# Performance work log

Hardware: AMD Instinct MI355X
Metric: run time of the kernel (lower is better)

Reference implementation:

```python
import jax, jax.numpy as jnp
import numpy as np

B, S, K, D = 512, 64, 8, 16
NE, NR, NU = 2_000_000, 64, 10_000
NSTEPS, NUNITS, NITER = 100, 128, 2


def _alpha_schedule():
    # betas = sigmoid(linspace(-6,6)) * (0.005 - 1e-5) + 1e-5; alphas_prod = cumprod(1-betas)
    betas = jax.nn.sigmoid(jnp.linspace(-6.0, 6.0, NSTEPS)) * (0.005 - 1e-5) + 1e-5
    aprod = jnp.cumprod(1.0 - betas)
    return jnp.sqrt(aprod), jnp.sqrt(1.0 - aprod)


def _forward(usr_emb, ent_emb, rel_emb, agg_W, agg_b, fc1_W, fc1_b, fc2_W, fc2_b,
             mlp_W1, mlp_b1, mlp_W2, mlp_b2, mlp_W3, mlp_b3, mlp_W4, mlp_b4,
             step_emb1, step_emb2, step_emb3, noise_e, u, v, click_seq, adj_ent, adj_rel, t):
    user = usr_emb[u]                                   # [B,D]
    # --- diffusion branch: x = x0*sqrt(abar_t) + e*sqrt(1-abar_t), then MLP with step-emb adds
    abar_sqrt, ombar_sqrt = _alpha_schedule()
    x = user * abar_sqrt[t][:, None] + noise_e * ombar_sqrt[t][:, None]
    for Wl, bl, se in ((mlp_W1, mlp_b1, step_emb1), (mlp_W2, mlp_b2, step_emb2), (mlp_W3, mlp_b3, step_emb3)):
        x = jax.nn.relu(x @ Wl + bl + se[t])            # [B,128]
    diff_out = x @ mlp_W4 + mlp_b4                      # [B,D]
    # --- multi-hop neighbor gather (entities/relations per hop)
    e0 = click_seq                                      # [B,S]
    e1 = adj_ent[e0]                                    # [B,S,K]
    e2 = adj_ent[e1].reshape(B, S, K * K)               # [B,S,K*K]
    r0 = adj_rel[e0]                                    # [B,S,K]
    r1 = adj_rel[e1].reshape(B, S, K * K)               # [B,S,K*K]
    ev = [ent_emb[e0][:, :, None, :], ent_emb[e1], ent_emb[e2]]  # [B,S,1,D],[B,S,K,D],[B,S,K*K,D]
    rv = [rel_emb[r0], rel_emb[r1]]

    def aggregate(self_v, neigh_v, rel_v, act):
        # KGCN sum-aggregator: user-relation score softmax over neighbors, weighted sum, linear, act
        scores = jnp.mean(user[:, None, None, None, :] * rel_v, axis=-1)   # [B,S,n,K]
        p = jax.nn.softmax(scores, axis=-1)
        neigh_agg = jnp.einsum('bsnk,bsnkd->bsnd', p, neigh_v)             # [B,S,n,D]
        return act((self_v + neigh_agg) @ agg_W + agg_b)

    for i in range(NITER):
        act = jnp.tanh if i == NITER - 1 else jax.nn.sigmoid
        nxt = []
        for hop in range(NITER - i):
            n_self = ev[hop].shape[2]
            nv = ev[hop + 1].reshape(B, S, n_self, K, D)
            relv = rv[hop].reshape(B, S, n_self, K, D)
            nxt.append(aggregate(ev[hop], nv, relv, act))
        ev = nxt
    item_emb = jax.nn.relu(ev[0].reshape(B, S, D))      # relu applied twice in source == once
    trans = item_emb                                    # Transform treated as identity (code unavailable)
    s_sum = jax.nn.relu(jnp.sum(trans, axis=1))         # [B,D]
    s_max = jax.nn.relu(jnp.max(trans, axis=1))         # [B,D]
    fusion = jnp.concatenate([s_sum, s_max], axis=1)    # [B,2D]
    feat = jax.nn.relu(jax.nn.relu(fusion @ fc1_W + fc1_b) @ fc2_W + fc2_b)  # [B,D]
    outs = jax.nn.sigmoid(jnp.sum(feat * ent_emb[v], axis=1))               # [B]
    return jnp.concatenate([outs[:, None], diff_out], axis=1)               # [B,1+D]


def setup_inputs() -> dict:
    key = jax.random.key(0)
    ks = iter(jax.random.split(key, 32))
    nrm = lambda shape, s: jax.random.normal(next(ks), shape, dtype=jnp.float32) * s
    zf = lambda shape: jnp.zeros(shape, dtype=jnp.float32)
    ri = lambda shape, hi: jax.random.randint(next(ks), shape, 0, hi, dtype=jnp.int32)
    return {
        'usr_emb': nrm((NU, D), 0.1), 'ent_emb': nrm((NE, D), 0.1), 'rel_emb': nrm((NR, D), 0.1),
        'agg_W': nrm((D, D), 0.25), 'agg_b': zf((D,)),
        'fc1_W': nrm((2 * D, 64), 0.18), 'fc1_b': zf((64,)),
        'fc2_W': nrm((64, D), 0.125), 'fc2_b': zf((D,)),
        'mlp_W1': nrm((D, NUNITS), 0.25), 'mlp_b1': zf((NUNITS,)),
        'mlp_W2': nrm((NUNITS, NUNITS), 0.09), 'mlp_b2': zf((NUNITS,)),
        'mlp_W3': nrm((NUNITS, NUNITS), 0.09), 'mlp_b3': zf((NUNITS,)),
        'mlp_W4': nrm((NUNITS, D), 0.09), 'mlp_b4': zf((D,)),
        'step_emb1': nrm((NSTEPS, NUNITS), 0.1), 'step_emb2': nrm((NSTEPS, NUNITS), 0.1),
        'step_emb3': nrm((NSTEPS, NUNITS), 0.1),
        'noise_e': jax.random.normal(next(ks), (B, D), dtype=jnp.float32),
        'u': ri((B,), NU), 'v': ri((B,), NE), 'click_seq': ri((B, S), NE),
        'adj_ent': ri((NE, K), NE), 'adj_rel': ri((NE, K), NR), 't': ri((B,), NSTEPS),
    }


def reference(usr_emb, ent_emb, rel_emb, agg_W, agg_b, fc1_W, fc1_b, fc2_W, fc2_b,
              mlp_W1, mlp_b1, mlp_W2, mlp_b2, mlp_W3, mlp_b3, mlp_W4, mlp_b4,
              step_emb1, step_emb2, step_emb3, noise_e, u, v, click_seq, adj_ent, adj_rel, t):
    return _forward(usr_emb, ent_emb, rel_emb, agg_W, agg_b, fc1_W, fc1_b, fc2_W, fc2_b,
                    mlp_W1, mlp_b1, mlp_W2, mlp_b2, mlp_W3, mlp_b3, mlp_W4, mlp_b4,
                    step_emb1, step_emb2, step_emb3, noise_e, u, v, click_seq, adj_ent, adj_rel, t)
```

## Files before the change

### kernel.cpp

```cpp
#include <hip/hip_runtime.h>
#include <math.h>

namespace {
constexpr int B = 512, S = 64, K = 8, D = 16, NR = 64, NSTEPS = 100, NUNITS = 128;
}

#define WAVE_LDS_FENCE() __asm__ volatile("s_waitcnt lgkmcnt(0)" ::: "memory")

__global__ __launch_bounds__(256) void k_prep_all(
    const float* __restrict__ usr_emb, const float* __restrict__ rel_emb,
    const int* __restrict__ u, const int* __restrict__ click_seq,
    const int* __restrict__ adj_ent, const int* __restrict__ adj_rel,
    float* __restrict__ w_tab, int* __restrict__ e1s, int* __restrict__ r0s,
    float* __restrict__ sa, float* __restrict__ so)
{
    int b = blockIdx.x, t = threadIdx.x;
    if (t < 64) {
        const float* ur = usr_emb + (long)u[b] * D;
        const float* rr = rel_emb + t * D;
        float s = 0.f;
#pragma unroll
        for (int d = 0; d < D; ++d) s += ur[d] * rr[d];
        w_tab[b * NR + t] = s * (1.0f / 16.0f);
    } else if (t < 128) {
        int p = b * S + (t - 64);
        int e0 = click_seq[p];
        const int4* ae = (const int4*)(adj_ent + (long)e0 * K);
        const int4* ar = (const int4*)(adj_rel + (long)e0 * K);
        int4 a0 = ae[0], a1 = ae[1], b0 = ar[0], b1 = ar[1];
        int4* oe = (int4*)(e1s + (long)p * K);
        int4* orr = (int4*)(r0s + (long)p * K);
        oe[0] = a0; oe[1] = a1;
        orr[0] = b0; orr[1] = b1;
    } else if (b == 0 && (t - 128) < NSTEPS) {
        int i = t - 128;
        float prod = 1.0f;
        for (int jj = 0; jj <= i; ++jj) {
            float x = -6.0f + (float)jj * (12.0f / 99.0f);
            float sig = 1.0f / (1.0f + expf(-x));
            prod *= (1.0f - (sig * (0.005f - 1e-5f) + 1e-5f));
        }
        sa[i] = sqrtf(prod);
        so[i] = sqrtf(1.0f - prod);
    }
}

__global__ __launch_bounds__(256) void k_kgcn(
    const float* __restrict__ ent_emb,
    const float* __restrict__ w_tab,
    const int* __restrict__ click_seq,
    const int* __restrict__ adj_ent,
    const int* __restrict__ adj_rel,
    const int* __restrict__ e1s,
    const int* __restrict__ r0s,
    const float* __restrict__ agg_W,
    const float* __restrict__ agg_b,
    float* __restrict__ item)
{
    __shared__ float wb[4][NR];
    __shared__ float Ws[4][D][D + 1];
    __shared__ float bs[4][D];
    __shared__ float Ms[4][K][D + 1];
    __shared__ float h1s[4][K][D + 1];
    __shared__ float h0s[4][D];
    __shared__ float A0s[4][D];
    __shared__ float M1s[4][D];
    __shared__ float p0s[4][K];

    const int tid = threadIdx.x;
    const int w = tid >> 6;
    const int lane = tid & 63;
    const int p = blockIdx.x * 4 + w;
    const int b = p >> 6;
    const int k = lane >> 3, j = lane & 7;

    const int e0 = click_seq[p];
    const int e1k = e1s[(long)p * K + k];
    const int r0k = r0s[(long)p * K + k];
    const int e2kj = adj_ent[(long)e1k * K + j];
    const int r1kj = adj_rel[(long)e1k * K + j];

    {
        const float4 wv = ((const float4*)agg_W)[lane];
        int row = lane >> 2, col = (lane & 3) * 4;
        Ws[w][row][col] = wv.x; Ws[w][row][col + 1] = wv.y;
        Ws[w][row][col + 2] = wv.z; Ws[w][row][col + 3] = wv.w;
        wb[w][lane] = w_tab[b * NR + lane];
        if (lane < D) bs[w][lane] = agg_b[lane];
    }
    WAVE_LDS_FENCE();

    float s1 = wb[w][r1kj];
    float m1 = s1;
    m1 = fmaxf(m1, __shfl_xor(m1, 1));
    m1 = fmaxf(m1, __shfl_xor(m1, 2));
    m1 = fmaxf(m1, __shfl_xor(m1, 4));
    float ex = expf(s1 - m1);
    float den = ex;
    den += __shfl_xor(den, 1);
    den += __shfl_xor(den, 2);
    den += __shfl_xor(den, 4);
    float p1 = ex / den;

    float q2r[D], q1r[D], q0r[D];
    {
        const float4* q2p = (const float4*)(ent_emb + (long)e2kj * D);
        float4 a0 = q2p[0], a1 = q2p[1], a2 = q2p[2], a3 = q2p[3];
        q2r[0]=a0.x; q2r[1]=a0.y; q2r[2]=a0.z; q2r[3]=a0.w;
        q2r[4]=a1.x; q2r[5]=a1.y; q2r[6]=a1.z; q2r[7]=a1.w;
        q2r[8]=a2.x; q2r[9]=a2.y; q2r[10]=a2.z; q2r[11]=a2.w;
        q2r[12]=a3.x; q2r[13]=a3.y; q2r[14]=a3.z; q2r[15]=a3.w;
    }
    {
        const float4* q1p = (const float4*)(ent_emb + (long)e1k * D);
        float4 a0 = q1p[0], a1 = q1p[1], a2 = q1p[2], a3 = q1p[3];
        q1r[0]=a0.x; q1r[1]=a0.y; q1r[2]=a0.z; q1r[3]=a0.w;
        q1r[4]=a1.x; q1r[5]=a1.y; q1r[6]=a1.z; q1r[7]=a1.w;
        q1r[8]=a2.x; q1r[9]=a2.y; q1r[10]=a2.z; q1r[11]=a2.w;
        q1r[12]=a3.x; q1r[13]=a3.y; q1r[14]=a3.z; q1r[15]=a3.w;
    }
    {
        const float4* q0p = (const float4*)(ent_emb + (long)e0 * D);
        float4 a0 = q0p[0], a1 = q0p[1], a2 = q0p[2], a3 = q0p[3];
        q0r[0]=a0.x; q0r[1]=a0.y; q0r[2]=a0.z; q0r[3]=a0.w;
        q0r[4]=a1.x; q0r[5]=a1.y; q0r[6]=a1.z; q0r[7]=a1.w;
        q0r[8]=a2.x; q0r[9]=a2.y; q0r[10]=a2.z; q0r[11]=a2.w;
        q0r[12]=a3.x; q0r[13]=a3.y; q0r[14]=a3.z; q0r[15]=a3.w;
    }

    {
        float cur[16];
#pragma unroll
        for (int d = 0; d < 16; ++d) cur[d] = p1 * q2r[d];
        const bool b0 = (lane & 1), b1 = (lane & 2), b2 = (lane & 4);
        float n8[8];
#pragma unroll
        for (int d = 0; d < 8; ++d) {
            float snd = b0 ? cur[d] : cur[d + 8];
            float kp  = b0 ? cur[d + 8] : cur[d];
            n8[d] = kp + __shfl_xor(snd, 1);
        }
        float n4[4];
#pragma unroll
        for (int d = 0; d < 4; ++d) {
            float snd = b1 ? n8[d] : n8[d + 4];
            float kp  = b1 ? n8[d + 4] : n8[d];
            n4[d] = kp + __shfl_xor(snd, 2);
        }
        float a0 = (b2 ? n4[2] : n4[0]) + __shfl_xor(b2 ? n4[0] : n4[2], 4);
        float a1 = (b2 ? n4[3] : n4[1]) + __shfl_xor(b2 ? n4[1] : n4[3], 4);
        const int dbase = (b0 ? 8 : 0) + (b1 ? 4 : 0) + (b2 ? 2 : 0);
        Ms[w][k][dbase]     = q1r[dbase]     + a0;
        Ms[w][k][dbase + 1] = q1r[dbase + 1] + a1;
    }

    float s0 = wb[w][r0k];
    float m0 = s0;
    m0 = fmaxf(m0, __shfl_xor(m0, 8));
    m0 = fmaxf(m0, __shfl_xor(m0, 16));
    m0 = fmaxf(m0, __shfl_xor(m0, 32));
    float e0x = expf(s0 - m0);
    float d0 = e0x;
    d0 += __shfl_xor(d0, 8);
    d0 += __shfl_xor(d0, 16);
    d0 += __shfl_xor(d0, 32);
    float p0 = e0x / d0;
    if (j == 0) p0s[w][k] = p0;

    {
        float cur[16];
#pragma unroll
        for (int d = 0; d < 16; ++d) cur[d] = p0 * q1r[d];
        const bool c0 = (lane & 8), c1 = (lane & 16), c2 = (lane & 32);
        float n8[8];
#pragma unroll
        for (int d = 0; d < 8; ++d) {
            float snd = c0 ? cur[d] : cur[d + 8];
            float kp  = c0 ? cur[d + 8] : cur[d];
            n8[d] = kp + __shfl_xor(snd, 8);
        }
        float n4[4];
#pragma unroll
        for (int d = 0; d < 4; ++d) {
            float snd = c1 ? n8[d] : n8[d + 4];
            float kp  = c1 ? n8[d + 4] : n8[d];
            n4[d] = kp + __shfl_xor(snd, 16);
        }
        float a0 = (c2 ? n4[2] : n4[0]) + __shfl_xor(c2 ? n4[0] : n4[2], 32);
        float a1 = (c2 ? n4[3] : n4[1]) + __shfl_xor(c2 ? n4[1] : n4[3], 32);
        const int dbase = (c0 ? 8 : 0) + (c1 ? 4 : 0) + (c2 ? 2 : 0);
        if (j == 0) { A0s[w][dbase] = a0; A0s[w][dbase + 1] = a1; }
    }
    WAVE_LDS_FENCE();

#pragma unroll
    for (int o = lane; o < 128; o += 64) {
        int ko = o >> 4, dd = o & 15;
        float acc = bs[w][dd];
#pragma unroll
        for (int din = 0; din < D; ++din) acc += Ms[w][ko][din] * Ws[w][din][dd];
        h1s[w][ko][dd] = 1.0f / (1.0f + expf(-acc));
    }

    const int ddl = lane & 15;
    {
        float acc = bs[w][ddl];
#pragma unroll
        for (int din = 0; din < D; ++din)
            acc += (q0r[din] + A0s[w][din]) * Ws[w][din][ddl];
        if (lane < D) h0s[w][lane] = 1.0f / (1.0f + expf(-acc));
    }
    WAVE_LDS_FENCE();

    if (lane < D) {
        float m = h0s[w][lane];
#pragma unroll
        for (int kk = 0; kk < K; ++kk) m += p0s[w][kk] * h1s[w][kk][lane];
        M1s[w][lane] = m;
    }
    WAVE_LDS_FENCE();

    {
        float acc = bs[w][ddl];
#pragma unroll
        for (int din = 0; din < D; ++din) acc += M1s[w][din] * Ws[w][din][ddl];
        if (lane < D) item[(long)p * D + lane] = fmaxf(tanhf(acc), 0.0f);
    }
}

__global__ __launch_bounds__(128) void k_tail(
    const float* __restrict__ item,
    const float* __restrict__ fc1_W, const float* __restrict__ fc1_b,
    const float* __restrict__ fc2_W, const float* __restrict__ fc2_b,
    const float* __restrict__ ent_emb, const int* __restrict__ v,
    const float* __restrict__ usr_emb, const float* __restrict__ noise_e,
    const int* __restrict__ u, const int* __restrict__ t_arr,
    const float* __restrict__ W1, const float* __restrict__ b1,
    const float* __restrict__ W2, const float* __restrict__ b2,
    const float* __restrict__ W3, const float* __restrict__ b3,
    const float* __restrict__ W4, const float* __restrict__ b4,
    const float* __restrict__ se1, const float* __restrict__ se2,
    const float* __restrict__ se3,
    const float* __restrict__ sa, const float* __restrict__ so,
    float* __restrict__ out)
{
    __shared__ float x0[D];
    __shared__ float ha[NUNITS];
    __shared__ float hb[NUNITS];
    __shared__ float sm[S][D + 1];
    __shared__ float fus[2 * D];
    __shared__ float hid[64];
    __shared__ float feat_s[D];

    int b = blockIdx.x, t = threadIdx.x;
    int ts = t_arr[b];

    if (t < D)
        x0[t] = usr_emb[(long)u[b] * D + t] * sa[ts] + noise_e[(long)b * D + t] * so[ts];
    __syncthreads();

    float a = b1[t] + se1[(long)ts * NUNITS + t];
#pragma unroll
    for (int i = 0; i < D; ++i) a += x0[i] * W1[i * NUNITS + t];
    ha[t] = fmaxf(a, 0.0f);
    __syncthreads();

    a = b2[t] + se2[(long)ts * NUNITS + t];
    for (int i = 0; i < NUNITS; ++i) a += ha[i] * W2[i * NUNITS + t];
    hb[t] = fmaxf(a, 0.0f);
    __syncthreads();

    a = b3[t] + se3[(long)ts * NUNITS + t];
    for (int i = 0; i < NUNITS; ++i) a += hb[i] * W3[i * NUNITS + t];
    __syncthreads();
    ha[t] = fmaxf(a, 0.0f);
    __syncthreads();

    if (t < D) {
        float acc = b4[t];
        for (int i = 0; i < NUNITS; ++i) acc += ha[i] * W4[i * D + t];
        out[(long)b * 17 + 1 + t] = acc;
    }

    if (t < 64) {
        const float4* ip = (const float4*)(item + ((long)b * S + t) * D);
        float4 r0 = ip[0], r1 = ip[1], r2 = ip[2], r3 = ip[3];
        sm[t][0]=r0.x;  sm[t][1]=r0.y;  sm[t][2]=r0.z;  sm[t][3]=r0.w;
        sm[t][4]=r1.x;  sm[t][5]=r1.y;  sm[t][6]=r1.z;  sm[t][7]=r1.w;
        sm[t][8]=r2.x;  sm[t][9]=r2.y;  sm[t][10]=r2.z; sm[t][11]=r2.w;
        sm[t][12]=r3.x; sm[t][13]=r3.y; sm[t][14]=r3.z; sm[t][15]=r3.w;
    }
    __syncthreads();

    if (t < D) {
        float sv = 0.0f, mv = -1e30f;
        for (int ss = 0; ss < S; ++ss) {
            float x = sm[ss][t];
            sv += x;
            mv = fmaxf(mv, x);
        }
        fus[t] = fmaxf(sv, 0.0f);
        fus[D + t] = fmaxf(mv, 0.0f);
    }
    __syncthreads();

    if (t < 64) {
        float acc = fc1_b[t];
#pragma unroll
        for (int i = 0; i < 2 * D; ++i) acc += fus[i] * fc1_W[i * 64 + t];
        hid[t] = fmaxf(acc, 0.0f);
    }
    __syncthreads();

    if (t < D) {
        float f = fc2_b[t];
#pragma unroll
        for (int i = 0; i < 64; ++i) f += hid[i] * fc2_W[i * D + t];
        feat_s[t] = fmaxf(f, 0.0f);
    }
    __syncthreads();

    if (t < D) {
        float g = feat_s[t] * ent_emb[(long)v[b] * D + t];
        g += __shfl_xor(g, 1);
        g += __shfl_xor(g, 2);
        g += __shfl_xor(g, 4);
        g += __shfl_xor(g, 8);
        if (t == 0) out[(long)b * 17] = 1.0f / (1.0f + expf(-g));
    }
}

extern "C" void kernel_launch(void* const* d_in, const int* in_sizes, int n_in,
                              void* d_out, int out_size, void* d_ws, size_t ws_size,
                              hipStream_t stream) {
    const float* usr_emb = (const float*)d_in[0];
    const float* ent_emb = (const float*)d_in[1];
    const float* rel_emb = (const float*)d_in[2];
    const float* agg_W   = (const float*)d_in[3];
    const float* agg_b   = (const float*)d_in[4];
    const float* fc1_W   = (const float*)d_in[5];
    const float* fc1_b   = (const float*)d_in[6];
    const float* fc2_W   = (const float*)d_in[7];
    const float* fc2_b   = (const float*)d_in[8];
    const float* mlp_W1  = (const float*)d_in[9];
    const float* mlp_b1  = (const float*)d_in[10];
    const float* mlp_W2  = (const float*)d_in[11];
    const float* mlp_b2  = (const float*)d_in[12];
    const float* mlp_W3  = (const float*)d_in[13];
    const float* mlp_b3  = (const float*)d_in[14];
    const float* mlp_W4  = (const float*)d_in[15];
    const float* mlp_b4  = (const float*)d_in[16];
    const float* se1     = (const float*)d_in[17];
    const float* se2     = (const float*)d_in[18];
    const float* se3     = (const float*)d_in[19];
    const float* noise_e = (const float*)d_in[20];
    const int* u         = (const int*)d_in[21];
    const int* v         = (const int*)d_in[22];
    const int* click_seq = (const int*)d_in[23];
    const int* adj_ent   = (const int*)d_in[24];
    const int* adj_rel   = (const int*)d_in[25];
    const int* t         = (const int*)d_in[26];
    float* out = (float*)d_out;

    float* ws = (float*)d_ws;
    float* w_tab = ws;
    float* sa    = w_tab + B * NR;
    float* so    = sa + 128;
    float* item  = so + 128;
    int*   e1s   = (int*)(item + B * S * D);
    int*   r0s   = e1s + B * S * K;

    k_prep_all<<<B, 256, 0, stream>>>(usr_emb, rel_emb, u, click_seq, adj_ent, adj_rel,
                                      w_tab, e1s, r0s, sa, so);
    k_kgcn<<<(B * S) / 4, 256, 0, stream>>>(ent_emb, w_tab, click_seq, adj_ent, adj_rel,
                                            e1s, r0s, agg_W, agg_b, item);
    k_tail<<<B, 128, 0, stream>>>(item, fc1_W, fc1_b, fc2_W, fc2_b, ent_emb, v,
                                  usr_emb, noise_e, u, t, mlp_W1, mlp_b1, mlp_W2, mlp_b2,
                                  mlp_W3, mlp_b3, mlp_W4, mlp_b4, se1, se2, se3, sa, so, out);
}
```

Measured before the change: 337.4 us.

## Prefetch packed second-hop neighbors in prep kernel and split tail MLP across 256 threads

The prep kernel now also gathers the second-hop adjacency rows for every first-hop neighbor and writes them as packed (entity<<6 | relation) ints. The KGCN kernel reads one coalesced int per lane instead of doing two dependent random gathers into adj_ent and adj_rel. Adjacency loads use nontemporal hints. The tail kernel doubles its threads to split the 128x128 matvecs in half and to overlap the fc branch with the diffusion MLP. The trade-off is extra workspace traffic and more work in the prep kernel.

Result: no change. 334.7 us (-0.8%).

```diff
diff --git a/kernel.cpp b/kernel.cpp
--- a/kernel.cpp
+++ b/kernel.cpp
@@ -3,6 +3,12 @@
 
 namespace {
 constexpr int B = 512, S = 64, K = 8, D = 16, NR = 64, NSTEPS = 100, NUNITS = 128;
+}
+
+typedef int i4 __attribute__((ext_vector_type(4)));
+
+static __device__ __forceinline__ i4 ntload4(const int* p) {
+    return __builtin_nontemporal_load((const i4*)p);
 }
 
 #define WAVE_LDS_FENCE() __asm__ volatile("s_waitcnt lgkmcnt(0)" ::: "memory")
@@ -12,8 +18,10 @@
     const int* __restrict__ u, const int* __restrict__ click_seq,
     const int* __restrict__ adj_ent, const int* __restrict__ adj_rel,
     float* __restrict__ w_tab, int* __restrict__ e1s, int* __restrict__ r0s,
+    int* __restrict__ e2r1,
     float* __restrict__ sa, float* __restrict__ so)
 {
+    __shared__ int e1L[S * K];
     int b = blockIdx.x, t = threadIdx.x;
     if (t < 64) {
         const float* ur = usr_emb + (long)u[b] * D;
@@ -23,15 +31,19 @@
         for (int d = 0; d < D; ++d) s += ur[d] * rr[d];
         w_tab[b * NR + t] = s * (1.0f / 16.0f);
     } else if (t < 128) {
-        int p = b * S + (t - 64);
+        int s = t - 64;
+        int p = b * S + s;
         int e0 = click_seq[p];
-        const int4* ae = (const int4*)(adj_ent + (long)e0 * K);
-        const int4* ar = (const int4*)(adj_rel + (long)e0 * K);
-        int4 a0 = ae[0], a1 = ae[1], b0 = ar[0], b1 = ar[1];
-        int4* oe = (int4*)(e1s + (long)p * K);
-        int4* orr = (int4*)(r0s + (long)p * K);
-        oe[0] = a0; oe[1] = a1;
-        orr[0] = b0; orr[1] = b1;
+        i4 a0 = ntload4(adj_ent + (long)e0 * K);
+        i4 a1 = ntload4(adj_ent + (long)e0 * K + 4);
+        i4 c0 = ntload4(adj_rel + (long)e0 * K);
+        i4 c1 = ntload4(adj_rel + (long)e0 * K + 4);
+        *(i4*)(e1s + (long)p * K)     = a0;
+        *(i4*)(e1s + (long)p * K + 4) = a1;
+        *(i4*)(r0s + (long)p * K)     = c0;
+        *(i4*)(r0s + (long)p * K + 4) = c1;
+        *(i4*)(e1L + s * K)     = a0;
+        *(i4*)(e1L + s * K + 4) = a1;
     } else if (b == 0 && (t - 128) < NSTEPS) {
         int i = t - 128;
         float prod = 1.0f;
@@ -43,16 +55,29 @@
         sa[i] = sqrtf(prod);
         so[i] = sqrtf(1.0f - prod);
     }
+    __syncthreads();
+
+    i4* oer = (i4*)(e2r1 + (long)b * (S * K * K));
+#pragma unroll
+    for (int it = 0; it < 2; ++it) {
+        int idx = t * 2 + it;
+        int e1k = e1L[idx];
+        i4 x0 = ntload4(adj_ent + (long)e1k * K);
+        i4 x1 = ntload4(adj_ent + (long)e1k * K + 4);
+        i4 y0 = ntload4(adj_rel + (long)e1k * K);
+        i4 y1 = ntload4(adj_rel + (long)e1k * K + 4);
+        oer[idx * 2]     = (x0 << 6) | y0;
+        oer[idx * 2 + 1] = (x1 << 6) | y1;
+    }
 }
 
 __global__ __launch_bounds__(256) void k_kgcn(
     const float* __restrict__ ent_emb,
     const float* __restrict__ w_tab,
     const int* __restrict__ click_seq,
-    const int* __restrict__ adj_ent,
-    const int* __restrict__ adj_rel,
     const int* __restrict__ e1s,
     const int* __restrict__ r0s,
+    const int* __restrict__ e2r1,
     const float* __restrict__ agg_W,
     const float* __restrict__ agg_b,
     float* __restrict__ item)
@@ -77,8 +102,9 @@
     const int e0 = click_seq[p];
     const int e1k = e1s[(long)p * K + k];
     const int r0k = r0s[(long)p * K + k];
-    const int e2kj = adj_ent[(long)e1k * K + j];
-    const int r1kj = adj_rel[(long)e1k * K + j];
+    const int pk = __builtin_nontemporal_load(e2r1 + (long)p * (K * K) + lane);
+    const int e2kj = ((unsigned)pk) >> 6;
+    const int r1kj = pk & 63;
 
     {
         const float4 wv = ((const float4*)agg_W)[lane];
@@ -228,7 +254,7 @@
     }
 }
 
-__global__ __launch_bounds__(128) void k_tail(
+__global__ __launch_bounds__(256) void k_tail(
     const float* __restrict__ item,
     const float* __restrict__ fc1_W, const float* __restrict__ fc1_b,
     const float* __restrict__ fc2_W, const float* __restrict__ fc2_b,
@@ -245,89 +271,107 @@
     float* __restrict__ out)
 {
     __shared__ float x0[D];
-    __shared__ float ha[NUNITS];
-    __shared__ float hb[NUNITS];
+    __shared__ float v1[NUNITS], v2[NUNITS], v3[NUNITS];
+    __shared__ float pp[2][NUNITS];
     __shared__ float sm[S][D + 1];
     __shared__ float fus[2 * D];
     __shared__ float hid[64];
     __shared__ float feat_s[D];
 
-    int b = blockIdx.x, t = threadIdx.x;
-    int ts = t_arr[b];
-
-    if (t < D)
-        x0[t] = usr_emb[(long)u[b] * D + t] * sa[ts] + noise_e[(long)b * D + t] * so[ts];
-    __syncthreads();
-
-    float a = b1[t] + se1[(long)ts * NUNITS + t];
-#pragma unroll
-    for (int i = 0; i < D; ++i) a += x0[i] * W1[i * NUNITS + t];
-    ha[t] = fmaxf(a, 0.0f);
-    __syncthreads();
-
-    a = b2[t] + se2[(long)ts * NUNITS + t];
-    for (int i = 0; i < NUNITS; ++i) a += ha[i] * W2[i * NUNITS + t];
-    hb[t] = fmaxf(a, 0.0f);
-    __syncthreads();
-
-    a = b3[t] + se3[(long)ts * NUNITS + t];
-    for (int i = 0; i < NUNITS; ++i) a += hb[i] * W3[i * NUNITS + t];
-    __syncthreads();
-    ha[t] = fmaxf(a, 0.0f);
-    __syncthreads();
-
-    if (t < D) {
-        float acc = b4[t];
-        for (int i = 0; i < NUNITS; ++i) acc += ha[i] * W4[i * D + t];
-        out[(long)b * 17 + 1 + t] = acc;
-    }
-
-    if (t < 64) {
-        const float4* ip = (const float4*)(item + ((long)b * S + t) * D);
+    const int b = blockIdx.x, tid = threadIdx.x;
+    const int t = tid & 127, h = tid >> 7;
+    const int ts = t_arr[b];
+
+    if (tid < D)
+        x0[tid] = usr_emb[(long)u[b] * D + tid] * sa[ts] + noise_e[(long)b * D + tid] * so[ts];
+    if (tid >= 128 && tid < 192) {
+        int ss = tid - 128;
+        const float4* ip = (const float4*)(item + ((long)b * S + ss) * D);
         float4 r0 = ip[0], r1 = ip[1], r2 = ip[2], r3 = ip[3];
-        sm[t][0]=r0.x;  sm[t][1]=r0.y;  sm[t][2]=r0.z;  sm[t][3]=r0.w;
-        sm[t][4]=r1.x;  sm[t][5]=r1.y;  sm[t][6]=r1.z;  sm[t][7]=r1.w;
-        sm[t][8]=r2.x;  sm[t][9]=r2.y;  sm[t][10]=r2.z; sm[t][11]=r2.w;
-        sm[t][12]=r3.x; sm[t][13]=r3.y; sm[t][14]=r3.z; sm[t][15]=r3.w;
-    }
-    __syncthreads();
-
-    if (t < D) {
+        sm[ss][0]=r0.x;  sm[ss][1]=r0.y;  sm[ss][2]=r0.z;  sm[ss][3]=r0.w;
+        sm[ss][4]=r1.x;  sm[ss][5]=r1.y;  sm[ss][6]=r1.z;  sm[ss][7]=r1.w;
+        sm[ss][8]=r2.x;  sm[ss][9]=r2.y;  sm[ss][10]=r2.z; sm[ss][11]=r2.w;
+        sm[ss][12]=r3.x; sm[ss][13]=r3.y; sm[ss][14]=r3.z; sm[ss][15]=r3.w;
+    }
+    __syncthreads();
+
+    if (h == 0) {
+        float a = b1[t] + se1[(long)ts * NUNITS + t];
+#pragma unroll
+        for (int i = 0; i < D; ++i) a += x0[i] * W1[i * NUNITS + t];
+        v1[t] = fmaxf(a, 0.0f);
+    } else if (tid >= 192 && tid < 192 + D) {
+        int d = tid - 192;
         float sv = 0.0f, mv = -1e30f;
+#pragma unroll
         for (int ss = 0; ss < S; ++ss) {
-            float x = sm[ss][t];
+            float x = sm[ss][d];
             sv += x;
             mv = fmaxf(mv, x);
         }
-        fus[t] = fmaxf(sv, 0.0f);
-        fus[D + t] = fmaxf(mv, 0.0f);
-    }
-    __syncthreads();
-
-    if (t < 64) {
-        float acc = fc1_b[t];
-#pragma unroll
-        for (int i = 0; i < 2 * D; ++i) acc += fus[i] * fc1_W[i * 64 + t];
-        hid[t] = fmaxf(acc, 0.0f);
-    }
-    __syncthreads();
-
-    if (t < D) {
-        float f = fc2_b[t];
-#pragma unroll
-        for (int i = 0; i < 64; ++i) f += hid[i] * fc2_W[i * D + t];
-        feat_s[t] = fmaxf(f, 0.0f);
-    }
-    __syncthreads();
-
-    if (t < D) {
-        float g = feat_s[t] * ent_emb[(long)v[b] * D + t];
-        g += __shfl_xor(g, 1);
-        g += __shfl_xor(g, 2);
-        g += __shfl_xor(g, 4);
-        g += __shfl_xor(g, 8);
-        if (t == 0) out[(long)b * 17] = 1.0f / (1.0f + expf(-g));
-    }
+        fus[d] = fmaxf(sv, 0.0f);
+        fus[D + d] = fmaxf(mv, 0.0f);
+    }
+    __syncthreads();
+
+    {
+        float part = 0.0f;
+        const float* wp = W2 + (long)(64 * h) * NUNITS + t;
+#pragma unroll 8
+        for (int i = 0; i < 64; ++i) part += v1[64 * h + i] * wp[(long)i * NUNITS];
+        pp[h][t] = part;
+    }
+    __syncthreads();
+
+    if (tid < NUNITS) {
+        v2[tid] = fmaxf(b2[tid] + se2[(long)ts * NUNITS + tid] + pp[0][tid] + pp[1][tid], 0.0f);
+    } else if (tid < 192) {
+        int o = tid - 128;
+        float acc = fc1_b[o];
+#pragma unroll
+        for (int i = 0; i < 2 * D; ++i) acc += fus[i] * fc1_W[i * 64 + o];
+        hid[o] = fmaxf(acc, 0.0f);
+    }
+    __syncthreads();
+
+    {
+        float part = 0.0f;
+        const float* wp = W3 + (long)(64 * h) * NUNITS + t;
+#pragma unroll 8
+        for (int i = 0; i < 64; ++i) part += v2[64 * h + i] * wp[(long)i * NUNITS];
+        pp[h][t] = part;
+    }
+    __syncthreads();
+
+    if (tid < NUNITS) {
+        v3[tid] = fmaxf(b3[tid] + se3[(long)ts * NUNITS + tid] + pp[0][tid] + pp[1][tid], 0.0f);
+    } else if (tid >= 192 && tid < 192 + D) {
+        int d = tid - 192;
+        float f = fc2_b[d];
+#pragma unroll
+        for (int i = 0; i < 64; ++i) f += hid[i] * fc2_W[i * D + d];
+        feat_s[d] = fmaxf(f, 0.0f);
+    }
+    __syncthreads();
+
+    if (tid < 32) {
+        int o = tid & 15, hh = tid >> 4;
+        float acc = 0.0f;
+#pragma unroll
+        for (int i = 0; i < 64; ++i) acc += v3[64 * hh + i] * W4[(64 * hh + i) * D + o];
+        pp[hh][o] = acc;
+    } else if (tid >= 192 && tid < 192 + D) {
+        int d = tid - 192;
+        float gv = feat_s[d] * ent_emb[(long)v[b] * D + d];
+        gv += __shfl_xor(gv, 1);
+        gv += __shfl_xor(gv, 2);
+        gv += __shfl_xor(gv, 4);
+        gv += __shfl_xor(gv, 8);
+        if (d == 0) out[(long)b * 17] = 1.0f / (1.0f + expf(-gv));
+    }
+    __syncthreads();
+
+    if (tid < D) out[(long)b * 17 + 1 + tid] = b4[tid] + pp[0][tid] + pp[1][tid];
 }
 
 extern "C" void kernel_launch(void* const* d_in, const int* in_sizes, int n_in,
@@ -369,12 +413,13 @@
     float* item  = so + 128;
     int*   e1s   = (int*)(item + B * S * D);
     int*   r0s   = e1s + B * S * K;
+    int*   e2r1  = r0s + B * S * K;
 
     k_prep_all<<<B, 256, 0, stream>>>(usr_emb, rel_emb, u, click_seq, adj_ent, adj_rel,
-                                      w_tab, e1s, r0s, sa, so);
-    k_kgcn<<<(B * S) / 4, 256, 0, stream>>>(ent_emb, w_tab, click_seq, adj_ent, adj_rel,
-                                            e1s, r0s, agg_W, agg_b, item);
-    k_tail<<<B, 128, 0, stream>>>(item, fc1_W, fc1_b, fc2_W, fc2_b, ent_emb, v,
+                                      w_tab, e1s, r0s, e2r1, sa, so);
+    k_kgcn<<<(B * S) / 4, 256, 0, stream>>>(ent_emb, w_tab, click_seq,
+                                            e1s, r0s, e2r1, agg_W, agg_b, item);
+    k_tail<<<B, 256, 0, stream>>>(item, fc1_W, fc1_b, fc2_W, fc2_b, ent_emb, v,
                                   usr_emb, noise_e, u, t, mlp_W1, mlp_b1, mlp_W2, mlp_b2,
                                   mlp_W3, mlp_b3, mlp_W4, mlp_b4, se1, se2, se3, sa, so, out);
 }
```

## Move diffusion MLP and second-hop adjacency gather into front kernel

Applied to the files above, without the earlier changes.

The prep kernel now also performs the second-hop adjacency gather. It writes e2 and r1 packed into one int per neighbour (entity<<6 | relation) using nontemporal loads, so k_kgcn reads one coalesced packed value instead of two dependent random gathers. The diffusion MLP moves from the tail kernel into extra blocks of the front kernel, with a split-K over two half-blocks, and the alpha schedule is computed per block. The tail becomes a single-wave kernel using wave-level LDS fences instead of barriers. The cost is an extra 1M-int workspace write, and the packing assumes entity ids fit in 26 bits and relation ids in 6 bits.

New measurement: 337.3 us. Within noise of the previous version (-0.0%).

```diff
diff --git a/kernel.cpp b/kernel.cpp
--- a/kernel.cpp
+++ b/kernel.cpp
@@ -5,54 +5,136 @@
 constexpr int B = 512, S = 64, K = 8, D = 16, NR = 64, NSTEPS = 100, NUNITS = 128;
 }
 
+typedef int i4 __attribute__((ext_vector_type(4)));
+
+static __device__ __forceinline__ i4 ntload4(const int* p) {
+    return __builtin_nontemporal_load((const i4*)p);
+}
+
 #define WAVE_LDS_FENCE() __asm__ volatile("s_waitcnt lgkmcnt(0)" ::: "memory")
 
-__global__ __launch_bounds__(256) void k_prep_all(
+__global__ __launch_bounds__(256) void k_front(
     const float* __restrict__ usr_emb, const float* __restrict__ rel_emb,
-    const int* __restrict__ u, const int* __restrict__ click_seq,
+    const int* __restrict__ u, const int* __restrict__ t_arr,
+    const int* __restrict__ click_seq,
     const int* __restrict__ adj_ent, const int* __restrict__ adj_rel,
+    const float* __restrict__ noise_e,
+    const float* __restrict__ W1, const float* __restrict__ b1,
+    const float* __restrict__ W2, const float* __restrict__ b2,
+    const float* __restrict__ W3, const float* __restrict__ b3,
+    const float* __restrict__ W4, const float* __restrict__ b4,
+    const float* __restrict__ se1, const float* __restrict__ se2,
+    const float* __restrict__ se3,
     float* __restrict__ w_tab, int* __restrict__ e1s, int* __restrict__ r0s,
-    float* __restrict__ sa, float* __restrict__ so)
+    int* __restrict__ e2r1, float* __restrict__ out)
 {
-    int b = blockIdx.x, t = threadIdx.x;
-    if (t < 64) {
-        const float* ur = usr_emb + (long)u[b] * D;
-        const float* rr = rel_emb + t * D;
+    __shared__ float ur[D], xn[D], bet[NSTEPS], x0[D];
+    __shared__ float v1[NUNITS], v2[NUNITS];
+    __shared__ float pp[2][NUNITS];
+
+    const int blk = blockIdx.x;
+    const int tid = threadIdx.x;
+
+    if (blk < 1024) {
+        const int unit = blk * 256 + tid;
+        const int p = unit >> 3, k = unit & 7;
+        const int e0 = click_seq[p];
+        const int e1k = __builtin_nontemporal_load(adj_ent + (long)e0 * K + k);
+        const int r0k = __builtin_nontemporal_load(adj_rel + (long)e0 * K + k);
+        e1s[unit] = e1k;
+        r0s[unit] = r0k;
+        i4 x0v = ntload4(adj_ent + (long)e1k * K);
+        i4 x1v = ntload4(adj_ent + (long)e1k * K + 4);
+        i4 y0v = ntload4(adj_rel + (long)e1k * K);
+        i4 y1v = ntload4(adj_rel + (long)e1k * K + 4);
+        i4* o = (i4*)(e2r1 + (long)unit * K);
+        o[0] = (x0v << 6) | y0v;
+        o[1] = (x1v << 6) | y1v;
+        return;
+    }
+
+    const int b = blk - 1024;
+    const int t = tid & 127, h = tid >> 7;
+    const int ts = t_arr[b];
+
+    if (tid < D) ur[tid] = usr_emb[(long)u[b] * D + tid];
+    else if (tid >= 32 && tid < 32 + D) xn[tid - 32] = noise_e[(long)b * D + (tid - 32)];
+    if (tid >= 64 && tid < 64 + NSTEPS) {
+        int i = tid - 64;
+        float x = -6.0f + (float)i * (12.0f / 99.0f);
+        float sig = 1.0f / (1.0f + expf(-x));
+        bet[i] = 1.0f - (sig * (0.005f - 1e-5f) + 1e-5f);
+    }
+    __syncthreads();
+
+    if (tid < D) {
+        float prod = 1.0f;
+        for (int i = 0; i <= ts; ++i) prod *= bet[i];
+        float sa_ = sqrtf(prod), so_ = sqrtf(1.0f - prod);
+        x0[tid] = ur[tid] * sa_ + xn[tid] * so_;
+    }
+    __syncthreads();
+
+    if (h == 0) {
+        float a = b1[t] + se1[(long)ts * NUNITS + t];
+#pragma unroll
+        for (int i = 0; i < D; ++i) a += x0[i] * W1[i * NUNITS + t];
+        v1[t] = fmaxf(a, 0.0f);
+    } else if (tid < 192) {
+        int r = tid - 128;
+        const float* rr = rel_emb + r * D;
         float s = 0.f;
 #pragma unroll
         for (int d = 0; d < D; ++d) s += ur[d] * rr[d];
-        w_tab[b * NR + t] = s * (1.0f / 16.0f);
-    } else if (t < 128) {
-        int p = b * S + (t - 64);
-        int e0 = click_seq[p];
-        const int4* ae = (const int4*)(adj_ent + (long)e0 * K);
-        const int4* ar = (const int4*)(adj_rel + (long)e0 * K);
-        int4 a0 = ae[0], a1 = ae[1], b0 = ar[0], b1 = ar[1];
-        int4* oe = (int4*)(e1s + (long)p * K);
-        int4* orr = (int4*)(r0s + (long)p * K);
-        oe[0] = a0; oe[1] = a1;
-        orr[0] = b0; orr[1] = b1;
-    } else if (b == 0 && (t - 128) < NSTEPS) {
-        int i = t - 128;
-        float prod = 1.0f;
-        for (int jj = 0; jj <= i; ++jj) {
-            float x = -6.0f + (float)jj * (12.0f / 99.0f);
-            float sig = 1.0f / (1.0f + expf(-x));
-            prod *= (1.0f - (sig * (0.005f - 1e-5f) + 1e-5f));
-        }
-        sa[i] = sqrtf(prod);
-        so[i] = sqrtf(1.0f - prod);
-    }
+        w_tab[b * NR + r] = s * (1.0f / 16.0f);
+    }
+    __syncthreads();
+
+    {
+        float part = 0.0f;
+        const float* wp = W2 + (long)(64 * h) * NUNITS + t;
+#pragma unroll 8
+        for (int i = 0; i < 64; ++i) part += v1[64 * h + i] * wp[(long)i * NUNITS];
+        pp[h][t] = part;
+    }
+    __syncthreads();
+
+    if (tid < NUNITS)
+        v2[tid] = fmaxf(b2[tid] + se2[(long)ts * NUNITS + tid] + pp[0][tid] + pp[1][tid], 0.0f);
+    __syncthreads();
+
+    {
+        float part = 0.0f;
+        const float* wp = W3 + (long)(64 * h) * NUNITS + t;
+#pragma unroll 8
+        for (int i = 0; i < 64; ++i) part += v2[64 * h + i] * wp[(long)i * NUNITS];
+        pp[h][t] = part;
+    }
+    __syncthreads();
+
+    if (tid < NUNITS)
+        v1[tid] = fmaxf(b3[tid] + se3[(long)ts * NUNITS + tid] + pp[0][tid] + pp[1][tid], 0.0f);
+    __syncthreads();
+
+    if (tid < 32) {
+        int o = tid & 15, hh = tid >> 4;
+        float acc = 0.0f;
+#pragma unroll
+        for (int i = 0; i < 64; ++i) acc += v1[64 * hh + i] * W4[(64 * hh + i) * D + o];
+        pp[hh][o] = acc;
+    }
+    __syncthreads();
+
+    if (tid < D) out[(long)b * 17 + 1 + tid] = b4[tid] + pp[0][tid] + pp[1][tid];
 }
 
 __global__ __launch_bounds__(256) void k_kgcn(
     const float* __restrict__ ent_emb,
     const float* __restrict__ w_tab,
     const int* __restrict__ click_seq,
-    const int* __restrict__ adj_ent,
-    const int* __restrict__ adj_rel,
     const int* __restrict__ e1s,
     const int* __restrict__ r0s,
+    const int* __restrict__ e2r1,
     const float* __restrict__ agg_W,
     const float* __restrict__ agg_b,
     float* __restrict__ item)
@@ -77,8 +159,9 @@
     const int e0 = click_seq[p];
     const int e1k = e1s[(long)p * K + k];
     const int r0k = r0s[(long)p * K + k];
-    const int e2kj = adj_ent[(long)e1k * K + j];
-    const int r1kj = adj_rel[(long)e1k * K + j];
+    const int pk = __builtin_nontemporal_load(e2r1 + (long)p * (K * K) + lane);
+    const int e2kj = ((unsigned)pk) >> 6;
+    const int r1kj = pk & 63;
 
     {
         const float4 wv = ((const float4*)agg_W)[lane];
@@ -228,61 +311,20 @@
     }
 }
 
-__global__ __launch_bounds__(128) void k_tail(
+__global__ __launch_bounds__(64) void k_back(
     const float* __restrict__ item,
     const float* __restrict__ fc1_W, const float* __restrict__ fc1_b,
     const float* __restrict__ fc2_W, const float* __restrict__ fc2_b,
     const float* __restrict__ ent_emb, const int* __restrict__ v,
-    const float* __restrict__ usr_emb, const float* __restrict__ noise_e,
-    const int* __restrict__ u, const int* __restrict__ t_arr,
-    const float* __restrict__ W1, const float* __restrict__ b1,
-    const float* __restrict__ W2, const float* __restrict__ b2,
-    const float* __restrict__ W3, const float* __restrict__ b3,
-    const float* __restrict__ W4, const float* __restrict__ b4,
-    const float* __restrict__ se1, const float* __restrict__ se2,
-    const float* __restrict__ se3,
-    const float* __restrict__ sa, const float* __restrict__ so,
     float* __restrict__ out)
 {
-    __shared__ float x0[D];
-    __shared__ float ha[NUNITS];
-    __shared__ float hb[NUNITS];
     __shared__ float sm[S][D + 1];
     __shared__ float fus[2 * D];
     __shared__ float hid[64];
-    __shared__ float feat_s[D];
-
-    int b = blockIdx.x, t = threadIdx.x;
-    int ts = t_arr[b];
-
-    if (t < D)
-        x0[t] = usr_emb[(long)u[b] * D + t] * sa[ts] + noise_e[(long)b * D + t] * so[ts];
-    __syncthreads();
-
-    float a = b1[t] + se1[(long)ts * NUNITS + t];
-#pragma unroll
-    for (int i = 0; i < D; ++i) a += x0[i] * W1[i * NUNITS + t];
-    ha[t] = fmaxf(a, 0.0f);
-    __syncthreads();
-
-    a = b2[t] + se2[(long)ts * NUNITS + t];
-    for (int i = 0; i < NUNITS; ++i) a += ha[i] * W2[i * NUNITS + t];
-    hb[t] = fmaxf(a, 0.0f);
-    __syncthreads();
-
-    a = b3[t] + se3[(long)ts * NUNITS + t];
-    for (int i = 0; i < NUNITS; ++i) a += hb[i] * W3[i * NUNITS + t];
-    __syncthreads();
-    ha[t] = fmaxf(a, 0.0f);
-    __syncthreads();
-
-    if (t < D) {
-        float acc = b4[t];
-        for (int i = 0; i < NUNITS; ++i) acc += ha[i] * W4[i * D + t];
-        out[(long)b * 17 + 1 + t] = acc;
-    }
-
-    if (t < 64) {
+
+    const int b = blockIdx.x, t = threadIdx.x;
+
+    {
         const float4* ip = (const float4*)(item + ((long)b * S + t) * D);
         float4 r0 = ip[0], r1 = ip[1], r2 = ip[2], r3 = ip[3];
         sm[t][0]=r0.x;  sm[t][1]=r0.y;  sm[t][2]=r0.z;  sm[t][3]=r0.w;
@@ -290,10 +332,11 @@
         sm[t][8]=r2.x;  sm[t][9]=r2.y;  sm[t][10]=r2.z; sm[t][11]=r2.w;
         sm[t][12]=r3.x; sm[t][13]=r3.y; sm[t][14]=r3.z; sm[t][15]=r3.w;
     }
-    __syncthreads();
+    WAVE_LDS_FENCE();
 
     if (t < D) {
         float sv = 0.0f, mv = -1e30f;
+#pragma unroll
         for (int ss = 0; ss < S; ++ss) {
             float x = sm[ss][t];
             sv += x;
@@ -302,26 +345,22 @@
         fus[t] = fmaxf(sv, 0.0f);
         fus[D + t] = fmaxf(mv, 0.0f);
     }
-    __syncthreads();
-
-    if (t < 64) {
+    WAVE_LDS_FENCE();
+
+    {
         float acc = fc1_b[t];
 #pragma unroll
         for (int i = 0; i < 2 * D; ++i) acc += fus[i] * fc1_W[i * 64 + t];
         hid[t] = fmaxf(acc, 0.0f);
     }
-    __syncthreads();
+    WAVE_LDS_FENCE();
 
     if (t < D) {
         float f = fc2_b[t];
 #pragma unroll
         for (int i = 0; i < 64; ++i) f += hid[i] * fc2_W[i * D + t];
-        feat_s[t] = fmaxf(f, 0.0f);
-    }
-    __syncthreads();
-
-    if (t < D) {
-        float g = feat_s[t] * ent_emb[(long)v[b] * D + t];
+        f = fmaxf(f, 0.0f);
+        float g = f * ent_emb[(long)v[b] * D + t];
         g += __shfl_xor(g, 1);
         g += __shfl_xor(g, 2);
         g += __shfl_xor(g, 4);
@@ -364,17 +403,16 @@
 
     float* ws = (float*)d_ws;
     float* w_tab = ws;
-    float* sa    = w_tab + B * NR;
-    float* so    = sa + 128;
-    float* item  = so + 128;
+    float* item  = w_tab + B * NR;
     int*   e1s   = (int*)(item + B * S * D);
     int*   r0s   = e1s + B * S * K;
-
-    k_prep_all<<<B, 256, 0, stream>>>(usr_emb, rel_emb, u, click_seq, adj_ent, adj_rel,
-                                      w_tab, e1s, r0s, sa, so);
-    k_kgcn<<<(B * S) / 4, 256, 0, stream>>>(ent_emb, w_tab, click_seq, adj_ent, adj_rel,
-                                            e1s, r0s, agg_W, agg_b, item);
-    k_tail<<<B, 128, 0, stream>>>(item, fc1_W, fc1_b, fc2_W, fc2_b, ent_emb, v,
-                                  usr_emb, noise_e, u, t, mlp_W1, mlp_b1, mlp_W2, mlp_b2,
-                                  mlp_W3, mlp_b3, mlp_W4, mlp_b4, se1, se2, se3, sa, so, out);
-}
+    int*   e2r1  = r0s + B * S * K;
+
+    k_front<<<1536, 256, 0, stream>>>(usr_emb, rel_emb, u, t, click_seq, adj_ent, adj_rel,
+                                      noise_e, mlp_W1, mlp_b1, mlp_W2, mlp_b2,
+                                      mlp_W3, mlp_b3, mlp_W4, mlp_b4, se1, se2, se3,
+                                      w_tab, e1s, r0s, e2r1, out);
+    k_kgcn<<<(B * S) / 4, 256, 0, stream>>>(ent_emb, w_tab, click_seq,
+                                            e1s, r0s, e2r1, agg_W, agg_b, item);
+    k_back<<<B, 64, 0, stream>>>(item, fc1_W, fc1_b, fc2_W, fc2_b, ent_emb, v, out);
+}
```
